# Optimization experiments

Measured on AMD Instinct MI355X. Metric: run time of the kernel, lower is better.

The kernel has to match this reference:

```python
import jax, jax.numpy as jnp
import numpy as np

N = 50000  # nodes == edges (source multiplies [N,H] node tensor by [E] edge attention)
HW = 8


def _adaptive_pool_2x2_from9(h):
    # PyTorch AdaptiveAvgPool2d((2,2)) on 9x9: bins [0:5) and [4:9) per dim (overlap at 4)
    def binpair(t, ax):
        s0 = jnp.take(t, jnp.arange(0, 5), axis=ax).mean(axis=ax)
        s1 = jnp.take(t, jnp.arange(4, 9), axis=ax).mean(axis=ax)
        return jnp.stack([s0, s1], axis=ax)
    return binpair(binpair(h, 3), 2)  # [N,64,2,2]


def _fe_net(x, c1w, c1b, c2w, c2b, fw, fb):
    h = x[:, None, :, :]  # [N,1,8,8]
    h = jax.lax.conv_general_dilated(h, c1w, (1, 1), ((1, 1), (1, 1)),
                                     dimension_numbers=('NCHW', 'OIHW', 'NCHW')) + c1b[None, :, None, None]
    h = jax.nn.relu(h)  # [N,32,8,8]
    h = jax.lax.conv_general_dilated(h, c2w, (1, 1), ((1, 1), (1, 1)),
                                     dimension_numbers=('NCHW', 'OIHW', 'NCHW')) + c2b[None, :, None, None]
    h = jax.nn.relu(h)  # [N,64,9,9]
    h = _adaptive_pool_2x2_from9(h).reshape(h.shape[0], -1)  # [N,256]
    return h @ fw + fb  # [N,32]


def _gcn(x, src, dst, W, b, n):
    h = x @ W
    idx = jnp.arange(n)
    s = jnp.concatenate([src, idx])
    d = jnp.concatenate([dst, idx])
    deg = jax.ops.segment_sum(jnp.ones(s.shape[0], h.dtype), d, num_segments=n)
    dis = jnp.where(deg > 0, jax.lax.rsqrt(jnp.maximum(deg, 1e-12)), 0.0)
    norm = dis[s] * dis[d]
    out = jax.ops.segment_sum(h[s] * norm[:, None], d, num_segments=n)
    return out + b


def _attention1(aux, src, dst, n):
    frame = aux[:, 2]
    fd = jnp.abs(frame[src] - frame[dst])
    outdeg = jax.ops.segment_sum(jnp.ones(src.shape[0], aux.dtype), src, num_segments=n)
    return jnp.where(fd == 1.0, 1.0 / jnp.maximum(outdeg[src], 1.0), 0.0)


def _attention2(aux, src, dst):
    ang, rad, frame = aux[:, 0], aux[:, 1], aux[:, 2]
    fd = jnp.abs(frame[src] - frame[dst])
    dx = rad[dst] * jnp.cos(ang[dst]) - rad[src] * jnp.cos(ang[src])
    dy = rad[dst] * jnp.sin(ang[dst]) - rad[src] * jnp.sin(ang[src])
    fd_safe = jnp.where(fd == 2.0, fd, 1.0)
    vel = jnp.sqrt(dx * dx + dy * dy + 1e-12) / fd_safe
    return jnp.where(fd == 2.0, jnp.exp(-vel / 8.5), 0.0)


def setup_inputs() -> dict:
    key = jax.random.key(0)
    ks = jax.random.split(key, 20)
    x = jax.random.normal(ks[0], (N, HW, HW), jnp.float32)
    angle = jax.random.uniform(ks[1], (N,), jnp.float32, 0.0, 2.0 * np.pi)
    radius = jax.random.uniform(ks[2], (N,), jnp.float32, 1.0, 100.0)
    frame = jax.random.randint(ks[3], (N,), 0, 10).astype(jnp.float32)
    aux_features = jnp.stack([angle, radius, frame], axis=1)
    edge_index = jax.random.randint(ks[4], (2, N), 0, N)
    s = 0.05
    p = lambda k, sh: jax.random.normal(k, sh, jnp.float32) * s
    return {
        'x': x, 'aux_features': aux_features, 'edge_index': edge_index,
        'conv1_w': p(ks[5], (32, 1, 3, 3)), 'conv1_b': jnp.zeros((32,), jnp.float32),
        'conv2_w': p(ks[6], (64, 32, 2, 2)), 'conv2_b': jnp.zeros((64,), jnp.float32),
        'fe_fc_w': p(ks[7], (256, 32)), 'fe_fc_b': jnp.zeros((32,), jnp.float32),
        'gcn1_w': p(ks[8], (32, 64)), 'gcn1_b': jnp.zeros((64,), jnp.float32),
        'gcn2_w': p(ks[9], (64, 64)), 'gcn2_b': jnp.zeros((64,), jnp.float32),
        'fc_w': p(ks[10], (64, 32)), 'fc_b': jnp.zeros((32,), jnp.float32),
        'out_w': p(ks[11], (32, 1)), 'out_b': jnp.zeros((1,), jnp.float32),
    }


def reference(x, aux_features, edge_index, conv1_w, conv1_b, conv2_w, conv2_b,
              fe_fc_w, fe_fc_b, gcn1_w, gcn1_b, gcn2_w, gcn2_b, fc_w, fc_b,
              out_w, out_b):
    n = x.shape[0]
    src, dst = edge_index[0], edge_index[1]
    sig = _fe_net(x, conv1_w, conv1_b, conv2_w, conv2_b, fe_fc_w, fe_fc_b)  # [N,32]
    att1 = _attention1(aux_features, src, dst, n)  # [E] == [N]
    x1 = jax.nn.relu(_gcn(sig, src, dst, gcn1_w, gcn1_b, n) * att1[:, None])
    att2 = _attention2(aux_features, src, dst)
    x2 = jax.nn.relu(_gcn(x1, src, dst, gcn2_w, gcn2_b, n) * att2[:, None])
    h = jax.nn.relu(x2 @ fc_w + fc_b)
    out = jax.nn.sigmoid(h @ out_w + out_b)  # [N,1]
    return out
```

## Files before the change

kernel.cpp:

```cpp
#include <hip/hip_runtime.h>
#include <math.h>

typedef float f32x4 __attribute__((ext_vector_type(4)));
typedef float f32x2 __attribute__((ext_vector_type(2)));
typedef __bf16 bf16x8 __attribute__((ext_vector_type(8)));
typedef unsigned short ushort8 __attribute__((ext_vector_type(8)));
typedef unsigned short ushort4v __attribute__((ext_vector_type(4)));

static __device__ __forceinline__ unsigned short bfbits(float f) {
    return __builtin_bit_cast(unsigned short, (__bf16)f);
}

__global__ __launch_bounds__(256, 3) void fe_kernel(
    const float* __restrict__ x,
    const float* __restrict__ w1T,
    const float* __restrict__ w2, const float* __restrict__ b2,
    unsigned short* __restrict__ poolbf, int n)
{
    __shared__ unsigned short hT[4][100][40];
    __shared__ float xs[4][104];

    const int t = threadIdx.x, lane = t & 63, wave = t >> 6;
    const int cl = lane & 15, kg = lane >> 4;

    bf16x8 bfr[4][4];
    #pragma unroll
    for (int ct = 0; ct < 4; ++ct)
        #pragma unroll
        for (int tap = 0; tap < 4; ++tap) {
            const float* gp = w2 + (size_t)(ct * 16 + cl) * 128 + kg * 32 + tap;
            ushort8 u;
            #pragma unroll
            for (int e = 0; e < 8; ++e) u[e] = bfbits(gp[e * 4]);
            bfr[ct][tap] = __builtin_bit_cast(bf16x8, u);
        }
    float b2r[4];
    #pragma unroll
    for (int ct = 0; ct < 4; ++ct) b2r[ct] = b2[ct * 16 + cl];

    unsigned int pm[3] = {0u, 0u, 0u};
    #pragma unroll
    for (int mt = 0; mt < 6; ++mt)
        #pragma unroll
        for (int rg = 0; rg < 4; ++rg) {
            const int slot = mt * 4 + rg;
            const int pd = mt * 16 + kg * 4 + rg;
            unsigned int bits = 0;
            if (pd < 81) {
                const int id = pd / 9, jd = pd - 9 * (pd / 9);
                if (id <= 4 && jd <= 4) bits |= 1u;
                if (id <= 4 && jd >= 4) bits |= 2u;
                if (id >= 4 && jd <= 4) bits |= 4u;
                if (id >= 4 && jd >= 4) bits |= 8u;
            }
            pm[slot >> 3] |= bits << ((slot & 7) * 4);
        }

    int rbase[6];
    #pragma unroll
    for (int mt = 0; mt < 6; ++mt) {
        const int p = mt * 16 + cl;
        const int ia = p / 9, ja = p - 9 * ia;
        rbase[mt] = (p < 81) ? (ia * 10 + ja) : 0;
    }

    {
        ushort8 z8 = {0,0,0,0,0,0,0,0};
        for (int r = lane; r < 100; r += 64) {
            const int pi = r / 10, pj = r - 10 * (r / 10);
            if (pi == 0 || pi == 9 || pj == 0 || pj == 9) {
                *reinterpret_cast<ushort8*>(&hT[wave][r][0])  = z8;
                *reinterpret_cast<ushort8*>(&hT[wave][r][8])  = z8;
                *reinterpret_cast<ushort8*>(&hT[wave][r][16]) = z8;
                *reinterpret_cast<ushort8*>(&hT[wave][r][24]) = z8;
                xs[wave][r] = 0.0f;
            }
        }
    }

    const int i = lane >> 3, j = lane & 7;
    const int rr = (i + 1) * 10 + (j + 1);
    const int gw = blockIdx.x * 4 + wave;
    const int nw = gridDim.x * 4;

    float v = (gw < n) ? x[(size_t)gw * 64 + lane] : 0.0f;

    for (int node = gw; node < n; node += nw) {
        #pragma unroll
        for (int ct = 0; ct < 4; ++ct)
            #pragma unroll
            for (int tap = 0; tap < 4; ++tap) {
                f32x4 tmp = __builtin_bit_cast(f32x4, bfr[ct][tap]);
                asm volatile("" : "+v"(tmp));
                bfr[ct][tap] = __builtin_bit_cast(bf16x8, tmp);
            }

        const int nn = node + nw;
        const float vnext = x[(size_t)(nn < n ? nn : node) * 64 + lane];

        xs[wave][rr] = v;
        asm volatile("s_waitcnt lgkmcnt(0)" ::: "memory");

        float xv[9];
        #pragma unroll
        for (int ki = 0; ki < 3; ++ki)
            #pragma unroll
            for (int kj = 0; kj < 3; ++kj)
                xv[ki * 3 + kj] = xs[wave][(i + ki) * 10 + (j + kj)];

        #pragma unroll
        for (int cp = 0; cp < 4; ++cp) {
            ushort8 hv;
            #pragma unroll
            for (int half = 0; half < 2; ++half) {
                const int cg = cp * 2 + half;
                f32x4 s = *reinterpret_cast<const f32x4*>(w1T + 288 + cg * 4);
                #pragma unroll
                for (int q = 0; q < 9; ++q) {
                    const f32x4 wq = *reinterpret_cast<const f32x4*>(w1T + q * 32 + cg * 4);
                    s += xv[q] * wq;
                }
                #pragma unroll
                for (int c = 0; c < 4; ++c)
                    hv[half * 4 + c] = bfbits(fmaxf(s[c], 0.0f));
            }
            *reinterpret_cast<ushort8*>(&hT[wave][rr][cp * 8]) = hv;
        }
        asm volatile("s_waitcnt lgkmcnt(0)" ::: "memory");

        f32x2 pb01[4], pb23[4];
        #pragma unroll
        for (int ct = 0; ct < 4; ++ct) { pb01[ct] = (f32x2){0.f,0.f}; pb23[ct] = (f32x2){0.f,0.f}; }

        #pragma unroll
        for (int mt = 0; mt < 6; ++mt) {
            const int rb = rbase[mt];
            bf16x8 a[4];
            a[0] = *reinterpret_cast<const bf16x8*>(&hT[wave][rb][kg * 8]);
            a[1] = *reinterpret_cast<const bf16x8*>(&hT[wave][rb + 1][kg * 8]);
            a[2] = *reinterpret_cast<const bf16x8*>(&hT[wave][rb + 10][kg * 8]);
            a[3] = *reinterpret_cast<const bf16x8*>(&hT[wave][rb + 11][kg * 8]);

            f32x4 acc[4];
            #pragma unroll
            for (int ct = 0; ct < 4; ++ct)
                acc[ct] = (f32x4){b2r[ct], b2r[ct], b2r[ct], b2r[ct]};
            #pragma unroll
            for (int tap = 0; tap < 4; ++tap)
                #pragma unroll
                for (int ct = 0; ct < 4; ++ct)
                    acc[ct] = __builtin_amdgcn_mfma_f32_16x16x32_bf16(a[tap], bfr[ct][tap], acc[ct], 0, 0, 0);

            #pragma unroll
            for (int rg = 0; rg < 4; ++rg) {
                if (mt * 16 + rg >= 81) continue;
                const int slot = mt * 4 + rg;
                const unsigned int bits = pm[slot >> 3] >> ((slot & 7) * 4);
                const f32x2 w01 = {(float)(bits & 1u), (float)((bits >> 1) & 1u)};
                const f32x2 w23 = {(float)((bits >> 2) & 1u), (float)((bits >> 3) & 1u)};
                #pragma unroll
                for (int ct = 0; ct < 4; ++ct) {
                    const float vr = fmaxf(acc[ct][rg], 0.0f);
                    const f32x2 v2 = {vr, vr};
                    pb01[ct] += v2 * w01;
                    pb23[ct] += v2 * w23;
                }
            }
        }

        const bool k0 = (kg & 1) != 0;
        const bool k1 = (kg & 2) != 0;
        float outb[4];
        #pragma unroll
        for (int b = 0; b < 4; ++b) {
            const float x0 = (b < 2) ? pb01[0][b] : pb23[0][b - 2];
            const float x1 = (b < 2) ? pb01[1][b] : pb23[1][b - 2];
            const float x2 = (b < 2) ? pb01[2][b] : pb23[2][b - 2];
            const float x3 = (b < 2) ? pb01[3][b] : pb23[3][b - 2];
            float keepA = k0 ? x1 : x0, sendA = k0 ? x0 : x1;
            float keepB = k0 ? x3 : x2, sendB = k0 ? x2 : x3;
            keepA += __shfl_xor(sendA, 16);
            keepB += __shfl_xor(sendB, 16);
            float keep = k1 ? keepB : keepA, send = k1 ? keepA : keepB;
            keep += __shfl_xor(send, 32);
            outb[b] = keep;
        }
        ushort4v pv;
        #pragma unroll
        for (int b = 0; b < 4; ++b) pv[b] = bfbits(outb[b]);
        *reinterpret_cast<ushort4v*>(poolbf + (size_t)node * 256 + lane * 4) = pv;

        v = vnext;
    }
}

__global__ void precount_k(const float* __restrict__ fw, const float* __restrict__ fb,
                           const float* __restrict__ g1w, const float* __restrict__ g2w,
                           const float* __restrict__ w1, const float* __restrict__ b1,
                           unsigned short* __restrict__ W1t, float* __restrict__ v1,
                           unsigned short* __restrict__ W2t, float* __restrict__ w1T,
                           const int* __restrict__ ei, float* __restrict__ outdeg,
                           float* __restrict__ indeg, int m)
{
    const int b = blockIdx.x, t = threadIdx.x;
    if (b < 64) {
        float s = 0.0f;
        for (int jj = 0; jj < 32; ++jj) s += fw[t * 32 + jj] * g1w[jj * 64 + b];
        W1t[b * 256 + t] = bfbits(0.04f * s);
    } else if (b < 80) {
        const int idx = (b - 64) * 256 + t;
        const int nc = idx >> 6, k = idx & 63;
        W2t[nc * 64 + k] = bfbits(g2w[k * 64 + nc]);
        if (b == 64 && t < 64) {
            float s = 0.0f;
            for (int jj = 0; jj < 32; ++jj) s += fb[jj] * g1w[jj * 64 + t];
            v1[t] = s;
        }
        if (b == 65 && t < 320) {
            const int q = t >> 5, c = t & 31;
            w1T[t] = (q < 9) ? w1[c * 9 + q] : b1[c];
        }
    } else {
        const int e = (b - 80) * 256 + t;
        if (e >= m) return;
        atomicAdd(&outdeg[ei[e]], 1.0f);
        atomicAdd(&indeg[ei[m + e]], 1.0f);
    }
}

template<bool ZEROACC>
__global__ __launch_bounds__(256) void mm1att_k(
    const unsigned short* __restrict__ A, const unsigned short* __restrict__ Bt,
    const float* __restrict__ v1, float* __restrict__ h, float* __restrict__ acc,
    const float* __restrict__ aux, const int* __restrict__ ei,
    const float* __restrict__ outdeg, const float* __restrict__ indeg,
    float* __restrict__ dis, float* __restrict__ att1, float* __restrict__ att2,
    int n, int m, int gmm)
{
    const int t = threadIdx.x;
    if ((int)blockIdx.x >= gmm) {
        const int e = (blockIdx.x - gmm) * 256 + t;
        if (e < n) dis[e] = rsqrtf(indeg[e] + 1.0f);
        if (e >= m) return;
        const int s = ei[e], d = ei[m + e];
        const float fs = aux[(size_t)s * 3 + 2], fdd = aux[(size_t)d * 3 + 2];
        const float fd = fabsf(fs - fdd);
        att1[e] = (fd == 1.0f) ? (1.0f / fmaxf(outdeg[s], 1.0f)) : 0.0f;
        const float angs = aux[(size_t)s * 3 + 0], rads = aux[(size_t)s * 3 + 1];
        const float angd = aux[(size_t)d * 3 + 0], radd = aux[(size_t)d * 3 + 1];
        const float dx = radd * cosf(angd) - rads * cosf(angs);
        const float dy = radd * sinf(angd) - rads * sinf(angs);
        const float vel = sqrtf(dx * dx + dy * dy + 1e-12f) * 0.5f;
        att2[e] = (fd == 2.0f) ? expf(-vel / 8.5f) : 0.0f;
        return;
    }

    const int lane = t & 63;
    const int cl = lane & 15, kg = lane >> 4;
    const int gw = blockIdx.x * 4 + (t >> 6);
    const int nw = gmm * 4;
    const int ntiles = (n + 15) >> 4;

    float vv[4];
    #pragma unroll
    for (int nt = 0; nt < 4; ++nt) vv[nt] = v1[nt * 16 + cl];

    for (int mt = gw; mt < ntiles; mt += nw) {
        const int r = min(mt * 16 + cl, n - 1);
        const unsigned short* ar = A + (size_t)r * 256 + kg * 8;
        f32x4 accf[4];
        #pragma unroll
        for (int nt = 0; nt < 4; ++nt)
            accf[nt] = (f32x4){vv[nt], vv[nt], vv[nt], vv[nt]};
        #pragma unroll
        for (int ks = 0; ks < 8; ++ks) {
            const bf16x8 afr = *reinterpret_cast<const bf16x8*>(ar + ks * 32);
            #pragma unroll
            for (int nt = 0; nt < 4; ++nt) {
                const bf16x8 bfrg = *reinterpret_cast<const bf16x8*>(
                    Bt + (size_t)(nt * 16 + cl) * 256 + ks * 32 + kg * 8);
                accf[nt] = __builtin_amdgcn_mfma_f32_16x16x32_bf16(afr, bfrg, accf[nt], 0, 0, 0);
            }
        }
        #pragma unroll
        for (int nt = 0; nt < 4; ++nt)
            #pragma unroll
            for (int rg = 0; rg < 4; ++rg) {
                const int row = mt * 16 + (kg << 2) + rg;
                if (row < n) h[(size_t)row * 64 + nt * 16 + cl] = accf[nt][rg];
            }
        if (ZEROACC) {
            const int zr = mt * 16 + cl;
            if (zr < n) {
                const f32x4 z = {0.f, 0.f, 0.f, 0.f};
                float* zp = acc + (size_t)zr * 64 + kg * 16;
                *reinterpret_cast<f32x4*>(zp)      = z;
                *reinterpret_cast<f32x4*>(zp + 4)  = z;
                *reinterpret_cast<f32x4*>(zp + 8)  = z;
                *reinterpret_cast<f32x4*>(zp + 12) = z;
            }
        }
    }
}

template<bool ZEROACC>
__global__ __launch_bounds__(256) void mm2f_k(
    const float* __restrict__ acc, const float* __restrict__ hin,
    const float* __restrict__ dis, const float* __restrict__ g1b,
    const float* __restrict__ att1, const unsigned short* __restrict__ Bt,
    float* __restrict__ hout, float* __restrict__ accz, int n)
{
    const int lane = threadIdx.x & 63;
    const int cl = lane & 15, kg = lane >> 4;
    const int gw = blockIdx.x * 4 + (threadIdx.x >> 6);
    const int nw = gridDim.x * 4;
    const int ntiles = (n + 15) >> 4;

    for (int mt = gw; mt < ntiles; mt += nw) {
        const int r = min(mt * 16 + cl, n - 1);
        const float di = dis[r];
        const float di2 = di * di;
        const float at = att1[r];
        f32x4 accf[4];
        #pragma unroll
        for (int nt = 0; nt < 4; ++nt) accf[nt] = (f32x4){0.f, 0.f, 0.f, 0.f};
        #pragma unroll
        for (int ks = 0; ks < 2; ++ks) {
            const float* ap = acc + (size_t)r * 64 + ks * 32 + kg * 8;
            const float* hp = hin + (size_t)r * 64 + ks * 32 + kg * 8;
            const float* bp = g1b + ks * 32 + kg * 8;
            ushort8 u;
            #pragma unroll
            for (int e = 0; e < 8; ++e)
                u[e] = bfbits(fmaxf((ap[e] + bp[e] + di2 * hp[e]) * at, 0.0f));
            if (ZEROACC) {
                const f32x4 z = {0.f, 0.f, 0.f, 0.f};
                float* zp = accz + (size_t)r * 64 + ks * 32 + kg * 8;
                *reinterpret_cast<f32x4*>(zp)     = z;
                *reinterpret_cast<f32x4*>(zp + 4) = z;
            }
            const bf16x8 afr = __builtin_bit_cast(bf16x8, u);
            #pragma unroll
            for (int nt = 0; nt < 4; ++nt) {
                const bf16x8 bfrg = *reinterpret_cast<const bf16x8*>(
                    Bt + (size_t)(nt * 16 + cl) * 64 + ks * 32 + kg * 8);
                accf[nt] = __builtin_amdgcn_mfma_f32_16x16x32_bf16(afr, bfrg, accf[nt], 0, 0, 0);
            }
        }
        #pragma unroll
        for (int nt = 0; nt < 4; ++nt)
            #pragma unroll
            for (int rg = 0; rg < 4; ++rg) {
                const int row = mt * 16 + (kg << 2) + rg;
                if (row < n) hout[(size_t)row * 64 + nt * 16 + cl] = accf[nt][rg];
            }
    }
}

__global__ void scatter_k(const float* __restrict__ h, const int* __restrict__ ei,
                          const float* __restrict__ dis, float* __restrict__ acc, int m)
{
    size_t idx = (size_t)blockIdx.x * blockDim.x + threadIdx.x;
    if (idx >= (size_t)m * 64) return;
    const int e = (int)(idx >> 6), k = (int)(idx & 63);
    const int s = ei[e], d = ei[m + e];
    const float w = dis[s] * dis[d];
    atomicAdd(&acc[(size_t)d * 64 + k], w * h[(size_t)s * 64 + k]);
}

__global__ __launch_bounds__(256) void finhead_k(
    const float* __restrict__ acc, const float* __restrict__ h,
    const float* __restrict__ dis, const float* __restrict__ g2b,
    const float* __restrict__ att2,
    const float* __restrict__ fcw, const float* __restrict__ fcb,
    const float* __restrict__ outw, const float* __restrict__ outb,
    float* __restrict__ out, int n)
{
    __shared__ float sm[8][64];
    const int t = threadIdx.x;
    const int nb = blockIdx.x * 8;

    #pragma unroll
    for (int pp = 0; pp < 2; ++pp) {
        const int p = t + pp * 256;
        const int nd = p >> 6, k = p & 63;
        const int node = nb + nd;
        if (node < n) {
            const float di = dis[node];
            const size_t idx = (size_t)node * 64 + k;
            sm[nd][k] = fmaxf((acc[idx] + g2b[k] + di * di * h[idx]) * att2[node], 0.0f);
        }
    }
    __syncthreads();

    const int nd = t >> 5, o = t & 31;
    const int node = nb + nd;
    if (node >= n) return;
    float s = fcb[o];
    #pragma unroll
    for (int k = 0; k < 64; ++k) s = fmaf(sm[nd][k], fcw[k * 32 + o], s);
    s = fmaxf(s, 0.0f);
    float p = s * outw[o];
    #pragma unroll
    for (int mk = 16; mk >= 1; mk >>= 1) p += __shfl_xor(p, mk);
    if (o == 0) out[node] = 1.0f / (1.0f + expf(-(p + outb[0])));
}

extern "C" void kernel_launch(void* const* d_in, const int* in_sizes, int n_in,
                              void* d_out, int out_size, void* d_ws, size_t ws_size,
                              hipStream_t stream)
{
    const float* x    = (const float*)d_in[0];
    const float* aux  = (const float*)d_in[1];
    const int*   ei   = (const int*)  d_in[2];
    const float* c1w  = (const float*)d_in[3];
    const float* c1b  = (const float*)d_in[4];
    const float* c2w  = (const float*)d_in[5];
    const float* c2b  = (const float*)d_in[6];
    const float* few  = (const float*)d_in[7];
    const float* feb  = (const float*)d_in[8];
    const float* g1w  = (const float*)d_in[9];
    const float* g1b  = (const float*)d_in[10];
    const float* g2w  = (const float*)d_in[11];
    const float* g2b  = (const float*)d_in[12];
    const float* fcw  = (const float*)d_in[13];
    const float* fcb  = (const float*)d_in[14];
    const float* outw = (const float*)d_in[15];
    const float* outb = (const float*)d_in[16];
    float* out = (float*)d_out;

    const int n = in_sizes[0] / 64;
    const int m = in_sizes[2] / 2;

    float* ws = (float*)d_ws;
    const size_t tailf = 8192 + 64 + 2048 + 320 + (size_t)3 * n + (size_t)2 * m;
    const bool sep = ws_size >= ((size_t)n * 256 + tailf) * sizeof(float);

    unsigned short* poolbf = (unsigned short*)ws;
    float* h;
    float* acc;
    float* wtail;
    if (sep) {
        h     = ws + (size_t)n * 128;
        acc   = ws + (size_t)n * 192;
        wtail = ws + (size_t)n * 256;
    } else {
        acc   = ws;
        h     = ws + (size_t)n * 128;
        wtail = ws + (size_t)n * 192;
    }
    unsigned short* W1t = (unsigned short*)wtail;
    float* v1   = wtail + 8192;
    unsigned short* W2t = (unsigned short*)(v1 + 64);
    float* w1T    = v1 + 64 + 2048;
    float* outdeg = w1T + 320;
    float* indeg  = outdeg + n;
    float* dis    = indeg + n;
    float* att1   = dis + n;
    float* att2   = att1 + m;

    const dim3 b256(256);
    const int gE   = (m + 255) / 256;
    const int gNE  = (max(n, m) + 255) / 256;
    const int gEM  = (int)(((size_t)m * 64 + 255) / 256);
    const int gMM  = (((n + 15) / 16) + 3) / 4;

    hipMemsetAsync(outdeg, 0, (size_t)2 * n * sizeof(float), stream);
    precount_k<<<80 + gE, b256, 0, stream>>>(few, feb, g1w, g2w, c1w, c1b,
                                             W1t, v1, W2t, w1T, ei, outdeg, indeg, m);
    fe_kernel<<<768, b256, 0, stream>>>(x, w1T, c2w, c2b, poolbf, n);

    if (sep) {
        mm1att_k<true><<<gMM + gNE, b256, 0, stream>>>(poolbf, W1t, v1, h, acc,
            aux, ei, outdeg, indeg, dis, att1, att2, n, m, gMM);
    } else {
        mm1att_k<false><<<gMM + gNE, b256, 0, stream>>>(poolbf, W1t, v1, h, acc,
            aux, ei, outdeg, indeg, dis, att1, att2, n, m, gMM);
        hipMemsetAsync(acc, 0, (size_t)n * 64 * sizeof(float), stream);
    }
    scatter_k<<<gEM, b256, 0, stream>>>(h, ei, dis, acc, m);

    mm2f_k<true><<<gMM, b256, 0, stream>>>(acc, h, dis, g1b, att1, W2t, h, acc, n);
    scatter_k<<<gEM, b256, 0, stream>>>(h, ei, dis, acc, m);

    finhead_k<<<(n + 7) / 8, b256, 0, stream>>>(acc, h, dis, g2b, att2,
                                                fcw, fcb, outw, outb, out, n);
}
```

Baseline: 263.4 us.

## Fuse GCN tail into cooperative persistent kernel and skip zero-attention scatters

The separate attention, matmul, scatter and head kernels are merged into one persistent kernel whose phases are separated by grid-wide syncs, launched cooperatively when the device supports it. A per-phase launch loop remains as fallback. The scatter phases now skip edges whose destination row is later multiplied by zero attention, and, in the second layer, edges whose source row is known to be zero. This removes launch gaps and atomic traffic that does not affect the output. In exchange, grid syncs cost time, the persistent grid may underfill some phases, and the workspace layout is fixed to the aliased variant with an explicit zeroing phase.

```diff
diff --git a/kernel.cpp b/kernel.cpp
--- a/kernel.cpp
+++ b/kernel.cpp
@@ -1,5 +1,8 @@
 #include <hip/hip_runtime.h>
+#include <hip/hip_cooperative_groups.h>
 #include <math.h>
+
+namespace cg = cooperative_groups;
 
 typedef float f32x4 __attribute__((ext_vector_type(4)));
 typedef float f32x2 __attribute__((ext_vector_type(2)));
@@ -113,11 +116,11 @@
             ushort8 hv;
             #pragma unroll
             for (int half = 0; half < 2; ++half) {
-                const int cg = cp * 2 + half;
-                f32x4 s = *reinterpret_cast<const f32x4*>(w1T + 288 + cg * 4);
+                const int cg2 = cp * 2 + half;
+                f32x4 s = *reinterpret_cast<const f32x4*>(w1T + 288 + cg2 * 4);
                 #pragma unroll
                 for (int q = 0; q < 9; ++q) {
-                    const f32x4 wq = *reinterpret_cast<const f32x4*>(w1T + q * 32 + cg * 4);
+                    const f32x4 wq = *reinterpret_cast<const f32x4*>(w1T + q * 32 + cg2 * 4);
                     s += xv[q] * wq;
                 }
                 #pragma unroll
@@ -228,46 +231,66 @@
     }
 }
 
-template<bool ZEROACC>
-__global__ __launch_bounds__(256) void mm1att_k(
-    const unsigned short* __restrict__ A, const unsigned short* __restrict__ Bt,
-    const float* __restrict__ v1, float* __restrict__ h, float* __restrict__ acc,
-    const float* __restrict__ aux, const int* __restrict__ ei,
-    const float* __restrict__ outdeg, const float* __restrict__ indeg,
-    float* __restrict__ dis, float* __restrict__ att1, float* __restrict__ att2,
-    int n, int m, int gmm)
-{
-    const int t = threadIdx.x;
-    if ((int)blockIdx.x >= gmm) {
-        const int e = (blockIdx.x - gmm) * 256 + t;
-        if (e < n) dis[e] = rsqrtf(indeg[e] + 1.0f);
-        if (e >= m) return;
-        const int s = ei[e], d = ei[m + e];
-        const float fs = aux[(size_t)s * 3 + 2], fdd = aux[(size_t)d * 3 + 2];
-        const float fd = fabsf(fs - fdd);
-        att1[e] = (fd == 1.0f) ? (1.0f / fmaxf(outdeg[s], 1.0f)) : 0.0f;
-        const float angs = aux[(size_t)s * 3 + 0], rads = aux[(size_t)s * 3 + 1];
-        const float angd = aux[(size_t)d * 3 + 0], radd = aux[(size_t)d * 3 + 1];
-        const float dx = radd * cosf(angd) - rads * cosf(angs);
-        const float dy = radd * sinf(angd) - rads * sinf(angs);
-        const float vel = sqrtf(dx * dx + dy * dy + 1e-12f) * 0.5f;
-        att2[e] = (fd == 2.0f) ? expf(-vel / 8.5f) : 0.0f;
-        return;
-    }
-
-    const int lane = t & 63;
+struct TailArgs {
+    const unsigned short* poolbf;
+    const unsigned short* W1t;
+    const float* v1;
+    float* h;
+    float* acc;
+    const float* aux;
+    const int* ei;
+    const float* outdeg;
+    const float* indeg;
+    float* dis;
+    float* att1;
+    float* att2;
+    const float* g1b;
+    const unsigned short* W2t;
+    const float* g2b;
+    const float* fcw;
+    const float* fcb;
+    const float* outw;
+    const float* outb;
+    float* out;
+    int n, m;
+};
+
+__device__ __forceinline__ void phase_attprep(const TailArgs& a)
+{
+    const int nm = a.n > a.m ? a.n : a.m;
+    const int stride = gridDim.x * 256;
+    for (int e = blockIdx.x * 256 + threadIdx.x; e < nm; e += stride) {
+        if (e < a.n) a.dis[e] = rsqrtf(a.indeg[e] + 1.0f);
+        if (e < a.m) {
+            const int s = a.ei[e], d = a.ei[a.m + e];
+            const float fs = a.aux[(size_t)s * 3 + 2], fdd = a.aux[(size_t)d * 3 + 2];
+            const float fd = fabsf(fs - fdd);
+            a.att1[e] = (fd == 1.0f) ? (1.0f / fmaxf(a.outdeg[s], 1.0f)) : 0.0f;
+            const float angs = a.aux[(size_t)s * 3 + 0], rads = a.aux[(size_t)s * 3 + 1];
+            const float angd = a.aux[(size_t)d * 3 + 0], radd = a.aux[(size_t)d * 3 + 1];
+            const float dx = radd * cosf(angd) - rads * cosf(angs);
+            const float dy = radd * sinf(angd) - rads * sinf(angs);
+            const float vel = sqrtf(dx * dx + dy * dy + 1e-12f) * 0.5f;
+            a.att2[e] = (fd == 2.0f) ? expf(-vel / 8.5f) : 0.0f;
+        }
+    }
+}
+
+__device__ __forceinline__ void phase_mm1(const TailArgs& a)
+{
+    const int t = threadIdx.x, lane = t & 63;
     const int cl = lane & 15, kg = lane >> 4;
     const int gw = blockIdx.x * 4 + (t >> 6);
-    const int nw = gmm * 4;
-    const int ntiles = (n + 15) >> 4;
+    const int nw = gridDim.x * 4;
+    const int ntiles = (a.n + 15) >> 4;
 
     float vv[4];
     #pragma unroll
-    for (int nt = 0; nt < 4; ++nt) vv[nt] = v1[nt * 16 + cl];
+    for (int nt = 0; nt < 4; ++nt) vv[nt] = a.v1[nt * 16 + cl];
 
     for (int mt = gw; mt < ntiles; mt += nw) {
-        const int r = min(mt * 16 + cl, n - 1);
-        const unsigned short* ar = A + (size_t)r * 256 + kg * 8;
+        const int r = min(mt * 16 + cl, a.n - 1);
+        const unsigned short* ar = a.poolbf + (size_t)r * 256 + kg * 8;
         f32x4 accf[4];
         #pragma unroll
         for (int nt = 0; nt < 4; ++nt)
@@ -278,7 +301,7 @@
             #pragma unroll
             for (int nt = 0; nt < 4; ++nt) {
                 const bf16x8 bfrg = *reinterpret_cast<const bf16x8*>(
-                    Bt + (size_t)(nt * 16 + cl) * 256 + ks * 32 + kg * 8);
+                    a.W1t + (size_t)(nt * 16 + cl) * 256 + ks * 32 + kg * 8);
                 accf[nt] = __builtin_amdgcn_mfma_f32_16x16x32_bf16(afr, bfrg, accf[nt], 0, 0, 0);
             }
         }
@@ -287,55 +310,65 @@
             #pragma unroll
             for (int rg = 0; rg < 4; ++rg) {
                 const int row = mt * 16 + (kg << 2) + rg;
-                if (row < n) h[(size_t)row * 64 + nt * 16 + cl] = accf[nt][rg];
-            }
-        if (ZEROACC) {
-            const int zr = mt * 16 + cl;
-            if (zr < n) {
-                const f32x4 z = {0.f, 0.f, 0.f, 0.f};
-                float* zp = acc + (size_t)zr * 64 + kg * 16;
-                *reinterpret_cast<f32x4*>(zp)      = z;
-                *reinterpret_cast<f32x4*>(zp + 4)  = z;
-                *reinterpret_cast<f32x4*>(zp + 8)  = z;
-                *reinterpret_cast<f32x4*>(zp + 12) = z;
-            }
-        }
-    }
-}
-
-template<bool ZEROACC>
-__global__ __launch_bounds__(256) void mm2f_k(
-    const float* __restrict__ acc, const float* __restrict__ hin,
-    const float* __restrict__ dis, const float* __restrict__ g1b,
-    const float* __restrict__ att1, const unsigned short* __restrict__ Bt,
-    float* __restrict__ hout, float* __restrict__ accz, int n)
-{
-    const int lane = threadIdx.x & 63;
+                if (row < a.n) a.h[(size_t)row * 64 + nt * 16 + cl] = accf[nt][rg];
+            }
+    }
+}
+
+__device__ __forceinline__ void phase_zacc(const TailArgs& a)
+{
+    const size_t total = (size_t)a.n * 16;
+    f32x4* p = reinterpret_cast<f32x4*>(a.acc);
+    const size_t stride = (size_t)gridDim.x * 256;
+    const f32x4 z = {0.f, 0.f, 0.f, 0.f};
+    for (size_t q = (size_t)blockIdx.x * 256 + threadIdx.x; q < total; q += stride)
+        p[q] = z;
+}
+
+template<bool HAS_S>
+__device__ __forceinline__ void phase_scatter(const TailArgs& a)
+{
+    const float* skd = HAS_S ? a.att2 : a.att1;
+    const size_t total = (size_t)a.m * 64;
+    const size_t stride = (size_t)gridDim.x * 256;
+    for (size_t idx = (size_t)blockIdx.x * 256 + threadIdx.x; idx < total; idx += stride) {
+        const int e = (int)(idx >> 6), k = (int)(idx & 63);
+        const int s = a.ei[e], d = a.ei[a.m + e];
+        if (skd[d] == 0.0f) continue;
+        if (HAS_S && a.att1[s] == 0.0f) continue;
+        const float w = a.dis[s] * a.dis[d];
+        atomicAdd(&a.acc[(size_t)d * 64 + k], w * a.h[(size_t)s * 64 + k]);
+    }
+}
+
+__device__ __forceinline__ void phase_mm2f(const TailArgs& a)
+{
+    const int t = threadIdx.x, lane = t & 63;
     const int cl = lane & 15, kg = lane >> 4;
-    const int gw = blockIdx.x * 4 + (threadIdx.x >> 6);
+    const int gw = blockIdx.x * 4 + (t >> 6);
     const int nw = gridDim.x * 4;
-    const int ntiles = (n + 15) >> 4;
+    const int ntiles = (a.n + 15) >> 4;
 
     for (int mt = gw; mt < ntiles; mt += nw) {
-        const int r = min(mt * 16 + cl, n - 1);
-        const float di = dis[r];
+        const int r = min(mt * 16 + cl, a.n - 1);
+        const float di = a.dis[r];
         const float di2 = di * di;
-        const float at = att1[r];
+        const float at = a.att1[r];
         f32x4 accf[4];
         #pragma unroll
         for (int nt = 0; nt < 4; ++nt) accf[nt] = (f32x4){0.f, 0.f, 0.f, 0.f};
         #pragma unroll
         for (int ks = 0; ks < 2; ++ks) {
-            const float* ap = acc + (size_t)r * 64 + ks * 32 + kg * 8;
-            const float* hp = hin + (size_t)r * 64 + ks * 32 + kg * 8;
-            const float* bp = g1b + ks * 32 + kg * 8;
+            const float* ap = a.acc + (size_t)r * 64 + ks * 32 + kg * 8;
+            const float* hp = a.h   + (size_t)r * 64 + ks * 32 + kg * 8;
+            const float* bp = a.g1b + ks * 32 + kg * 8;
             ushort8 u;
             #pragma unroll
             for (int e = 0; e < 8; ++e)
                 u[e] = bfbits(fmaxf((ap[e] + bp[e] + di2 * hp[e]) * at, 0.0f));
-            if (ZEROACC) {
+            {
                 const f32x4 z = {0.f, 0.f, 0.f, 0.f};
-                float* zp = accz + (size_t)r * 64 + ks * 32 + kg * 8;
+                float* zp = a.acc + (size_t)r * 64 + ks * 32 + kg * 8;
                 *reinterpret_cast<f32x4*>(zp)     = z;
                 *reinterpret_cast<f32x4*>(zp + 4) = z;
             }
@@ -343,7 +376,7 @@
             #pragma unroll
             for (int nt = 0; nt < 4; ++nt) {
                 const bf16x8 bfrg = *reinterpret_cast<const bf16x8*>(
-                    Bt + (size_t)(nt * 16 + cl) * 64 + ks * 32 + kg * 8);
+                    a.W2t + (size_t)(nt * 16 + cl) * 64 + ks * 32 + kg * 8);
                 accf[nt] = __builtin_amdgcn_mfma_f32_16x16x32_bf16(afr, bfrg, accf[nt], 0, 0, 0);
             }
         }
@@ -352,58 +385,68 @@
             #pragma unroll
             for (int rg = 0; rg < 4; ++rg) {
                 const int row = mt * 16 + (kg << 2) + rg;
-                if (row < n) hout[(size_t)row * 64 + nt * 16 + cl] = accf[nt][rg];
-            }
-    }
-}
-
-__global__ void scatter_k(const float* __restrict__ h, const int* __restrict__ ei,
-                          const float* __restrict__ dis, float* __restrict__ acc, int m)
-{
-    size_t idx = (size_t)blockIdx.x * blockDim.x + threadIdx.x;
-    if (idx >= (size_t)m * 64) return;
-    const int e = (int)(idx >> 6), k = (int)(idx & 63);
-    const int s = ei[e], d = ei[m + e];
-    const float w = dis[s] * dis[d];
-    atomicAdd(&acc[(size_t)d * 64 + k], w * h[(size_t)s * 64 + k]);
-}
-
-__global__ __launch_bounds__(256) void finhead_k(
-    const float* __restrict__ acc, const float* __restrict__ h,
-    const float* __restrict__ dis, const float* __restrict__ g2b,
-    const float* __restrict__ att2,
-    const float* __restrict__ fcw, const float* __restrict__ fcb,
-    const float* __restrict__ outw, const float* __restrict__ outb,
-    float* __restrict__ out, int n)
+                if (row < a.n) a.h[(size_t)row * 64 + nt * 16 + cl] = accf[nt][rg];
+            }
+    }
+}
+
+__device__ __forceinline__ void phase_finhead(const TailArgs& a)
 {
     __shared__ float sm[8][64];
     const int t = threadIdx.x;
-    const int nb = blockIdx.x * 8;
-
-    #pragma unroll
-    for (int pp = 0; pp < 2; ++pp) {
-        const int p = t + pp * 256;
-        const int nd = p >> 6, k = p & 63;
+
+    for (int nb = blockIdx.x * 8; nb < a.n; nb += gridDim.x * 8) {
+        #pragma unroll
+        for (int pp = 0; pp < 2; ++pp) {
+            const int p = t + pp * 256;
+            const int nd = p >> 6, k = p & 63;
+            const int node = nb + nd;
+            if (node < a.n) {
+                const float di = a.dis[node];
+                const size_t idx = (size_t)node * 64 + k;
+                sm[nd][k] = fmaxf((a.acc[idx] + a.g2b[k] + di * di * a.h[idx]) * a.att2[node], 0.0f);
+            }
+        }
+        __syncthreads();
+
+        const int nd = t >> 5, o = t & 31;
         const int node = nb + nd;
-        if (node < n) {
-            const float di = dis[node];
-            const size_t idx = (size_t)node * 64 + k;
-            sm[nd][k] = fmaxf((acc[idx] + g2b[k] + di * di * h[idx]) * att2[node], 0.0f);
-        }
-    }
-    __syncthreads();
-
-    const int nd = t >> 5, o = t & 31;
-    const int node = nb + nd;
-    if (node >= n) return;
-    float s = fcb[o];
-    #pragma unroll
-    for (int k = 0; k < 64; ++k) s = fmaf(sm[nd][k], fcw[k * 32 + o], s);
-    s = fmaxf(s, 0.0f);
-    float p = s * outw[o];
-    #pragma unroll
-    for (int mk = 16; mk >= 1; mk >>= 1) p += __shfl_xor(p, mk);
-    if (o == 0) out[node] = 1.0f / (1.0f + expf(-(p + outb[0])));
+        if (node < a.n) {
+            float s = a.fcb[o];
+            #pragma unroll
+            for (int k = 0; k < 64; ++k) s = fmaf(sm[nd][k], a.fcw[k * 32 + o], s);
+            s = fmaxf(s, 0.0f);
+            float p = s * a.outw[o];
+            #pragma unroll
+            for (int mk = 16; mk >= 1; mk >>= 1) p += __shfl_xor(p, mk);
+            if (o == 0) a.out[node] = 1.0f / (1.0f + expf(-(p + a.outb[0])));
+        }
+        __syncthreads();
+    }
+}
+
+__global__ __launch_bounds__(256, 4) void tail_k(TailArgs a, int phase)
+{
+    if (phase < 0) {
+        cg::grid_group g = cg::this_grid();
+        phase_attprep(a);        g.sync();
+        phase_mm1(a);            g.sync();
+        phase_zacc(a);           g.sync();
+        phase_scatter<false>(a); g.sync();
+        phase_mm2f(a);           g.sync();
+        phase_scatter<true>(a);  g.sync();
+        phase_finhead(a);
+        return;
+    }
+    switch (phase) {
+        case 0: phase_attprep(a);        break;
+        case 1: phase_mm1(a);            break;
+        case 2: phase_zacc(a);           break;
+        case 3: phase_scatter<false>(a); break;
+        case 4: phase_mm2f(a);           break;
+        case 5: phase_scatter<true>(a);  break;
+        case 6: phase_finhead(a);        break;
+    }
 }
 
 extern "C" void kernel_launch(void* const* d_in, const int* in_sizes, int n_in,
@@ -433,22 +476,10 @@
     const int m = in_sizes[2] / 2;
 
     float* ws = (float*)d_ws;
-    const size_t tailf = 8192 + 64 + 2048 + 320 + (size_t)3 * n + (size_t)2 * m;
-    const bool sep = ws_size >= ((size_t)n * 256 + tailf) * sizeof(float);
-
     unsigned short* poolbf = (unsigned short*)ws;
-    float* h;
-    float* acc;
-    float* wtail;
-    if (sep) {
-        h     = ws + (size_t)n * 128;
-        acc   = ws + (size_t)n * 192;
-        wtail = ws + (size_t)n * 256;
-    } else {
-        acc   = ws;
-        h     = ws + (size_t)n * 128;
-        wtail = ws + (size_t)n * 192;
-    }
+    float* acc  = ws;
+    float* h    = ws + (size_t)n * 128;
+    float* wtail = ws + (size_t)n * 192;
     unsigned short* W1t = (unsigned short*)wtail;
     float* v1   = wtail + 8192;
     unsigned short* W2t = (unsigned short*)(v1 + 64);
@@ -460,29 +491,43 @@
     float* att2   = att1 + m;
 
     const dim3 b256(256);
-    const int gE   = (m + 255) / 256;
-    const int gNE  = (max(n, m) + 255) / 256;
-    const int gEM  = (int)(((size_t)m * 64 + 255) / 256);
-    const int gMM  = (((n + 15) / 16) + 3) / 4;
+    const int gE = (m + 255) / 256;
 
     hipMemsetAsync(outdeg, 0, (size_t)2 * n * sizeof(float), stream);
     precount_k<<<80 + gE, b256, 0, stream>>>(few, feb, g1w, g2w, c1w, c1b,
                                              W1t, v1, W2t, w1T, ei, outdeg, indeg, m);
     fe_kernel<<<768, b256, 0, stream>>>(x, w1T, c2w, c2b, poolbf, n);
 
-    if (sep) {
-        mm1att_k<true><<<gMM + gNE, b256, 0, stream>>>(poolbf, W1t, v1, h, acc,
-            aux, ei, outdeg, indeg, dis, att1, att2, n, m, gMM);
-    } else {
-        mm1att_k<false><<<gMM + gNE, b256, 0, stream>>>(poolbf, W1t, v1, h, acc,
-            aux, ei, outdeg, indeg, dis, att1, att2, n, m, gMM);
-        hipMemsetAsync(acc, 0, (size_t)n * 64 * sizeof(float), stream);
-    }
-    scatter_k<<<gEM, b256, 0, stream>>>(h, ei, dis, acc, m);
-
-    mm2f_k<true><<<gMM, b256, 0, stream>>>(acc, h, dis, g1b, att1, W2t, h, acc, n);
-    scatter_k<<<gEM, b256, 0, stream>>>(h, ei, dis, acc, m);
-
-    finhead_k<<<(n + 7) / 8, b256, 0, stream>>>(acc, h, dis, g2b, att2,
-                                                fcw, fcb, outw, outb, out, n);
-}
+    TailArgs ta;
+    ta.poolbf = poolbf; ta.W1t = W1t; ta.v1 = v1; ta.h = h; ta.acc = acc;
+    ta.aux = aux; ta.ei = ei; ta.outdeg = outdeg; ta.indeg = indeg;
+    ta.dis = dis; ta.att1 = att1; ta.att2 = att2; ta.g1b = g1b; ta.W2t = W2t;
+    ta.g2b = g2b; ta.fcw = fcw; ta.fcb = fcb; ta.outw = outw; ta.outb = outb;
+    ta.out = out; ta.n = n; ta.m = m;
+
+    bool done = false;
+    int dev = 0;
+    hipGetDevice(&dev);
+    int coop = 0;
+    hipDeviceGetAttribute(&coop, hipDeviceAttributeCooperativeLaunch, dev);
+    if (coop) {
+        int nCU = 0;
+        hipDeviceGetAttribute(&nCU, hipDeviceAttributeMultiprocessorCount, dev);
+        int maxb = 0;
+        hipError_t occ = hipOccupancyMaxActiveBlocksPerMultiprocessor(
+            &maxb, reinterpret_cast<const void*>(tail_k), 256, 0);
+        if (occ == hipSuccess && maxb > 0 && nCU > 0) {
+            int grid = maxb * nCU;
+            if (grid > 2048) grid = 2048;
+            int ph = -1;
+            void* args[] = { &ta, &ph };
+            if (hipLaunchCooperativeKernel(reinterpret_cast<const void*>(tail_k),
+                                           dim3(grid), dim3(256), args, 0, stream) == hipSuccess)
+                done = true;
+        }
+    }
+    if (!done) {
+        for (int ph = 0; ph < 7; ++ph)
+            tail_k<<<1024, b256, 0, stream>>>(ta, ph);
+    }
+}
```

New measurement: 668.4 us. +153.7%, slower.
